# Performance work log

Hardware: AMD Instinct MI355X
Metric: run time of the kernel (lower is better)

Reference implementation:

```python
import jax, jax.numpy as jnp
import numpy as np

V, D, B, L = 100000, 64, 4096, 200

def setup_inputs() -> dict:
    key = jax.random.key(0)
    ks = jax.random.split(key, 10)
    s = 0.05  # keep activations in a sane range for sigmoid
    return {
        "item_ids": jax.random.randint(ks[0], (B,), 0, V),
        "history": jax.random.randint(ks[1], (B, L), 0, V),
        "hist_len": jax.random.randint(ks[2], (B,), 1, L + 1),
        "emb_table": jax.random.normal(ks[3], (V, D), jnp.float32) * s,
        "aW1": jax.random.normal(ks[4], (3 * D, D), jnp.float32) * s,
        "ab1": jnp.zeros((D,), jnp.float32),
        "aW2": jax.random.normal(ks[5], (D, 1), jnp.float32) * s,
        "ab2": jnp.zeros((1,), jnp.float32),
        "fW1": jax.random.normal(ks[6], (3 * D, 128), jnp.float32) * s,
        "fb1": jnp.zeros((128,), jnp.float32),
        "fW2": jax.random.normal(ks[7], (128, 64), jnp.float32) * s,
        "fb2": jnp.zeros((64,), jnp.float32),
        "fW3": jax.random.normal(ks[8], (64, 1), jnp.float32) * s,
        "fb3": jnp.zeros((1,), jnp.float32),
    }

def reference(item_ids, history, hist_len, emb_table, aW1, ab1, aW2, ab2,
              fW1, fb1, fW2, fb2, fW3, fb3):
    target = emb_table[item_ids]                      # [B, D]
    hist = emb_table[history]                         # [B, L, D]
    # original pads short histories with zero rows -> zero the padded tail
    mask = (jnp.arange(hist.shape[1])[None, :] < hist_len[:, None]).astype(hist.dtype)
    hist = hist * mask[..., None]
    tgt = jnp.broadcast_to(target[:, None, :], hist.shape)     # [B, L, D]
    # attention_fc takes 3*D features: (hist, target, hist*target)
    feat = jnp.concatenate([hist, tgt, hist * tgt], axis=-1)   # [B, L, 3D]
    h = jax.nn.relu(feat @ aW1 + ab1)                 # [B, L, D]
    scores = (h @ aW2 + ab2)[..., 0]                  # [B, L]
    # faithful to original: softmax over full padded length (no length mask)
    w = jax.nn.softmax(scores, axis=1)
    pooled = jnp.einsum('bl,bld->bd', w, hist)        # [B, D]
    comb = jnp.concatenate([target, pooled, pooled - target], axis=-1)  # [B, 3D]
    z = jax.nn.relu(comb @ fW1 + fb1)
    z = jax.nn.relu(z @ fW2 + fb2)
    return jax.nn.sigmoid(z @ fW3 + fb3)              # [B, 1]
```

## Files before the change

kernel.cpp:

```cpp
#include <hip/hip_runtime.h>
#include <hip/hip_bf16.h>

#define NV 100000
#define ND 64
#define NB 4096
#define NL 200
#define MT 13

typedef __bf16 bf16_t;
typedef __bf16 bf16x8 __attribute__((ext_vector_type(8)));
typedef __bf16 bf16x4 __attribute__((ext_vector_type(4)));
typedef float f32x4 __attribute__((ext_vector_type(4)));

#define TB_ELEMS ((long)NV * ND)
#define TBV (TB_ELEMS / 8)
#define FT1 (128 * 192)
#define FT2 (64 * 128)
#define CVT_TASKS (TBV + FT1 + FT2)

__global__ __launch_bounds__(256)
void cvt_kernel(const float* __restrict__ emb,
                const float* __restrict__ fW1,
                const float* __restrict__ fW2,
                bf16_t* __restrict__ tb,
                bf16_t* __restrict__ fW1T,
                bf16_t* __restrict__ fW2T)
{
    long t = (long)blockIdx.x * 256 + threadIdx.x;
    if (t >= CVT_TASKS) return;
    if (t < TBV) {
        long i = t * 8;
        f32x4 a0 = *(const f32x4*)(emb + i);
        f32x4 a1 = *(const f32x4*)(emb + i + 4);
        bf16x8 o;
#pragma unroll
        for (int j = 0; j < 4; ++j) { o[j] = (bf16_t)a0[j]; o[j + 4] = (bf16_t)a1[j]; }
        *(bf16x8*)(tb + i) = o;
    } else {
        int u = (int)(t - TBV);
        if (u < FT1) {
            int n = u / 192, k = u - n * 192;
            fW1T[u] = (bf16_t)fW1[k * 128 + n];
        } else {
            int u2 = u - FT1;
            int n = u2 >> 7, k = u2 & 127;
            fW2T[u2] = (bf16_t)fW2[k * 64 + n];
        }
    }
}

__global__ __launch_bounds__(512, 4)
void din_kernel1(const int* __restrict__ item_ids,
                 const int* __restrict__ history,
                 const int* __restrict__ hist_len,
                 const float* __restrict__ emb,
                 const bf16_t* __restrict__ tb,
                 const float* __restrict__ aW1,
                 const float* __restrict__ ab1,
                 const float* __restrict__ aW2,
                 const bf16_t* __restrict__ fW1T, const float* __restrict__ fb1,
                 const bf16_t* __restrict__ fW2T, const float* __restrict__ fb2,
                 const float* __restrict__ fW3, const float* __restrict__ fb3,
                 float* __restrict__ out)
{
    __shared__ __align__(16) bf16_t histA[2][208 * 64];
    __shared__ __align__(16) bf16_t wbT[2][64 * 64];
    __shared__ float tgt[2][64];
    __shared__ __align__(16) float scores[2][208];
    __shared__ float wts[2][208];
    __shared__ float pp2[2][512];
    __shared__ float red[2][8];
    __shared__ float cb2[2][64];

    bf16_t* comb16 = (bf16_t*)wbT;
    bf16_t* z1s    = (bf16_t*)wbT + 3200;
    float*  z2f    = (float*)((bf16_t*)wbT + 5376);

    const int b0  = blockIdx.x * 2;
    const int tid = threadIdx.x;
    const int len0 = hist_len[b0];
    const int len1 = hist_len[b0 + 1];

    if (tid < 128) {
        int bx = tid >> 6, d = tid & 63;
        tgt[bx][d] = emb[(long)item_ids[b0 + bx] * ND + d];
    }

    {
        const int p = tid & 1;
        const int s = tid >> 1;
        const int bxA = (s >= 208);
        const int lA  = s - bxA * 208;
        const int lB  = s + 48;
        const int lenA = bxA ? len1 : len0;
        const bool vB = (s < 160);
        const bf16x8 z = (bf16x8)(bf16_t)0.f;
        bf16x8 a0 = z, a1 = z, a2 = z, a3 = z;
        bf16x8 c0 = z, c1 = z, c2 = z, c3 = z;
        if (lA < lenA) {
            const bf16_t* src = tb + (long)history[(long)(b0 + bxA) * NL + lA] * ND + p * 32;
            a0 = *(const bf16x8*)(src);
            a1 = *(const bf16x8*)(src + 8);
            a2 = *(const bf16x8*)(src + 16);
            a3 = *(const bf16x8*)(src + 24);
        }
        if (vB && lB < len1) {
            const bf16_t* src = tb + (long)history[(long)(b0 + 1) * NL + lB] * ND + p * 32;
            c0 = *(const bf16x8*)(src);
            c1 = *(const bf16x8*)(src + 8);
            c2 = *(const bf16x8*)(src + 16);
            c3 = *(const bf16x8*)(src + 24);
        }
        {
            bf16_t* d = &histA[bxA][lA * 64];
            const int S = (lA & 7) << 3;
            *(bf16x8*)&d[(p * 32 +  0) ^ S] = a0;
            *(bf16x8*)&d[(p * 32 +  8) ^ S] = a1;
            *(bf16x8*)&d[(p * 32 + 16) ^ S] = a2;
            *(bf16x8*)&d[(p * 32 + 24) ^ S] = a3;
        }
        if (vB) {
            bf16_t* d = &histA[1][lB * 64];
            const int S = (lB & 7) << 3;
            *(bf16x8*)&d[(p * 32 +  0) ^ S] = c0;
            *(bf16x8*)&d[(p * 32 +  8) ^ S] = c1;
            *(bf16x8*)&d[(p * 32 + 16) ^ S] = c2;
            *(bf16x8*)&d[(p * 32 + 24) ^ S] = c3;
        }
    }

    {
        const int n  = tid & 63;
        const int kp = tid >> 6;
        const long t0 = (long)item_ids[b0] * ND;
        const long t1 = (long)item_ids[b0 + 1] * ND;
        f32x4 tk0a = *(const f32x4*)(emb + t0 + kp * 8);
        f32x4 tk0b = *(const f32x4*)(emb + t0 + kp * 8 + 4);
        f32x4 tk1a = *(const f32x4*)(emb + t1 + kp * 8);
        f32x4 tk1b = *(const f32x4*)(emb + t1 + kp * 8 + 4);
        float cs0 = 0.f, cs1 = 0.f;
        bf16x8 w0v, w1v;
#pragma unroll
        for (int i = 0; i < 8; ++i) {
            int k = kp * 8 + i;
            float tk0 = (i < 4) ? tk0a[i] : tk0b[i - 4];
            float tk1 = (i < 4) ? tk1a[i] : tk1b[i - 4];
            float ah = aW1[k * 64 + n];
            float am = aW1[(64 + k) * 64 + n];
            float ap = aW1[(128 + k) * 64 + n];
            w0v[i] = (bf16_t)(ah + tk0 * ap);
            w1v[i] = (bf16_t)(ah + tk1 * ap);
            cs0 += tk0 * am;
            cs1 += tk1 * am;
        }
        const int S = (n & 7) << 3;
        *(bf16x8*)&wbT[0][n * 64 + ((kp * 8) ^ S)] = w0v;
        *(bf16x8*)&wbT[1][n * 64 + ((kp * 8) ^ S)] = w1v;
        pp2[0][kp * 64 + n] = cs0;
        pp2[1][kp * 64 + n] = cs1;
    }
    __syncthreads();

    if (tid < 128) {
        const int bx = tid >> 6, n = tid & 63;
        float s = ab1[n];
#pragma unroll
        for (int kp = 0; kp < 8; ++kp) s += pp2[bx][kp * 64 + n];
        cb2[bx][n] = s;
    }
    __syncthreads();

    {
        const int wave = tid >> 6;
        const int lane = tid & 63;
        const int bx   = wave & 1;
        const int col  = lane & 15;
        const int quad = lane >> 4;

        bf16x8 afrag[4][2];
#pragma unroll
        for (int nt = 0; nt < 4; ++nt) {
            const int n = nt * 16 + col;
            const int S = (n & 7) << 3;
#pragma unroll
            for (int kb = 0; kb < 2; ++kb)
                afrag[nt][kb] = *(const bf16x8*)&wbT[bx][n * 64 + ((kb * 32 + quad * 8) ^ S)];
        }
        float cv[4][4], a2[4][4];
#pragma unroll
        for (int nt = 0; nt < 4; ++nt)
#pragma unroll
            for (int i = 0; i < 4; ++i) {
                const int no = nt * 16 + quad * 4 + i;
                cv[nt][i] = cb2[bx][no];
                a2[nt][i] = aW2[no];
            }

        for (int mt = (wave >> 1); mt < MT; mt += 4) {
            const int l = mt * 16 + col;
            const int S = (l & 7) << 3;
            const bf16_t* base = &histA[bx][l * 64];
            bf16x8 bf0 = *(const bf16x8*)&base[(     quad * 8) ^ S];
            bf16x8 bf1 = *(const bf16x8*)&base[(32 + quad * 8) ^ S];
            float sc = 0.f;
#pragma unroll
            for (int nt = 0; nt < 4; ++nt) {
                f32x4 acc = {0.f, 0.f, 0.f, 0.f};
                acc = __builtin_amdgcn_mfma_f32_16x16x32_bf16(afrag[nt][0], bf0, acc, 0, 0, 0);
                acc = __builtin_amdgcn_mfma_f32_16x16x32_bf16(afrag[nt][1], bf1, acc, 0, 0, 0);
#pragma unroll
                for (int i = 0; i < 4; ++i) {
                    float h = acc[i] + cv[nt][i];
                    h = h > 0.f ? h : 0.f;
                    sc += h * a2[nt][i];
                }
            }
            sc += __shfl_xor(sc, 16, 64);
            sc += __shfl_xor(sc, 32, 64);
            if (quad == 0) scores[bx][mt * 16 + col] = sc;
        }
    }
    __syncthreads();

    {
        const int bx = tid >> 8, t = tid & 255;
        float s = (t < NL) ? scores[bx][t] : -1e30f;
        float m = s;
        for (int off = 32; off > 0; off >>= 1) m = fmaxf(m, __shfl_xor(m, off, 64));
        if ((t & 63) == 0) red[bx][t >> 6] = m;
        __syncthreads();
        m = fmaxf(fmaxf(red[bx][0], red[bx][1]), fmaxf(red[bx][2], red[bx][3]));
        float e = (t < NL) ? __expf(s - m) : 0.f;
        if (t < NL) wts[bx][t] = e;
        else if (t < 208) wts[bx][t] = 0.f;
        float ss = e;
        for (int off = 32; off > 0; off >>= 1) ss += __shfl_xor(ss, off, 64);
        if ((t & 63) == 0) red[bx][4 + (t >> 6)] = ss;
        __syncthreads();
    }

    {
        const int bx = tid >> 8, t = tid & 255;
        const int c = t & 15;
        const int g = t >> 4;
        const int w4 = (tid >> 6) & 3;
        const float rtot = 1.f / (red[bx][4] + red[bx][5] + red[bx][6] + red[bx][7]);
        f32x4 acc = {0.f, 0.f, 0.f, 0.f};
#pragma unroll
        for (int j = 0; j < 13; ++j) {
            const int l = g + j * 16;
            const float wl = wts[bx][l];
            bf16x4 v = *(const bf16x4*)&histA[bx][l * 64 + ((c * 4) ^ ((l & 7) << 3))];
#pragma unroll
            for (int k = 0; k < 4; ++k) acc[k] += wl * (float)v[k];
        }
#pragma unroll
        for (int k = 0; k < 4; ++k) {
            acc[k] += __shfl_xor(acc[k], 16, 64);
            acc[k] += __shfl_xor(acc[k], 32, 64);
            acc[k] *= rtot;
        }
        if ((tid & 63) < 16) *(f32x4*)&pp2[bx][w4 * 64 + c * 4] = acc;
    }

    bf16x8 bw1[6]; float b1v;
    bf16x8 bw2[4]; float b2v = 0.f;
    {
        const int wave = tid >> 6, lane = tid & 63;
        const int col = lane & 15, quad = lane >> 4;
        const int n = wave * 16 + col;
#pragma unroll
        for (int ks = 0; ks < 6; ++ks)
            bw1[ks] = *(const bf16x8*)&fW1T[(long)n * 192 + ks * 32 + quad * 8];
        b1v = fb1[n];
        if (wave < 4) {
            const int n2 = wave * 16 + col;
#pragma unroll
            for (int ks = 0; ks < 4; ++ks)
                bw2[ks] = *(const bf16x8*)&fW2T[(long)n2 * 128 + ks * 32 + quad * 8];
            b2v = fb2[n2];
        }
    }
    __syncthreads();

    {
        const int bx = tid >> 8, t = tid & 255;
        if (t < 192) {
            const int d = t & 63;
            float v;
            if (t < 64) v = tgt[bx][d];
            else {
                float pl = pp2[bx][d] + pp2[bx][64 + d] + pp2[bx][128 + d] + pp2[bx][192 + d];
                v = (t < 128) ? pl : pl - tgt[bx][d];
            }
            comb16[bx * 200 + t] = (bf16_t)v;
        }
        if (tid >= 384) {
            const bf16x8 z = (bf16x8)(bf16_t)0.f;
            const int u = tid - 384;
#pragma unroll
            for (int s = u; s < 350; s += 128) *(bf16x8*)&comb16[400 + s * 8] = z;
        }
    }
    __syncthreads();

    {
        const int wave = tid >> 6, lane = tid & 63;
        const int col = lane & 15, quad = lane >> 4;
        f32x4 acc = {0.f, 0.f, 0.f, 0.f};
#pragma unroll
        for (int ks = 0; ks < 6; ++ks) {
            bf16x8 a = *(const bf16x8*)&comb16[col * 200 + ks * 32 + quad * 8];
            acc = __builtin_amdgcn_mfma_f32_16x16x32_bf16(a, bw1[ks], acc, 0, 0, 0);
        }
        const int n = wave * 16 + col;
#pragma unroll
        for (int i = 0; i < 4; ++i) {
            const int m = quad * 4 + i;
            float zv = (m < 2) ? fmaxf(acc[i] + b1v, 0.f) : 0.f;
            z1s[m * 136 + n] = (bf16_t)zv;
        }
    }
    __syncthreads();

    {
        const int wave = tid >> 6, lane = tid & 63;
        const int col = lane & 15, quad = lane >> 4;
        if (wave < 4) {
            f32x4 acc = {0.f, 0.f, 0.f, 0.f};
#pragma unroll
            for (int ks = 0; ks < 4; ++ks) {
                bf16x8 a = *(const bf16x8*)&z1s[col * 136 + ks * 32 + quad * 8];
                acc = __builtin_amdgcn_mfma_f32_16x16x32_bf16(a, bw2[ks], acc, 0, 0, 0);
            }
            const int n2 = wave * 16 + col;
#pragma unroll
            for (int i = 0; i < 4; ++i) {
                const int m = quad * 4 + i;
                if (m < 2) z2f[m * 64 + n2] = fmaxf(acc[i] + b2v, 0.f);
            }
        }
    }
    __syncthreads();

    if (tid < 128) {
        const int bx = tid >> 6, j = tid & 63;
        float s = z2f[bx * 64 + j] * fW3[j];
        for (int off = 32; off > 0; off >>= 1) s += __shfl_xor(s, off, 64);
        if (j == 0) out[b0 + bx] = 1.f / (1.f + __expf(-(s + fb3[0])));
    }
}

extern "C" void kernel_launch(void* const* d_in, const int* in_sizes, int n_in,
                              void* d_out, int out_size, void* d_ws, size_t ws_size,
                              hipStream_t stream) {
    const int*   item_ids = (const int*)d_in[0];
    const int*   history  = (const int*)d_in[1];
    const int*   hist_len = (const int*)d_in[2];
    const float* emb      = (const float*)d_in[3];
    const float* aW1      = (const float*)d_in[4];
    const float* ab1      = (const float*)d_in[5];
    const float* aW2      = (const float*)d_in[6];
    const float* fW1      = (const float*)d_in[8];
    const float* fb1      = (const float*)d_in[9];
    const float* fW2      = (const float*)d_in[10];
    const float* fb2      = (const float*)d_in[11];
    const float* fW3      = (const float*)d_in[12];
    const float* fb3      = (const float*)d_in[13];

    bf16_t* tb   = (bf16_t*)d_ws;
    bf16_t* fW1T = tb + TB_ELEMS;
    bf16_t* fW2T = fW1T + FT1;

    cvt_kernel<<<(int)((CVT_TASKS + 255) / 256), 256, 0, stream>>>(emb, fW1, fW2,
                                                                   tb, fW1T, fW2T);
    din_kernel1<<<NB / 2, 512, 0, stream>>>(item_ids, history, hist_len, emb, tb,
                                            aW1, ab1, aW2,
                                            fW1T, fb1, fW2T, fb2, fW3, fb3,
                                            (float*)d_out);
}
```

Baseline: 140.1 us.

## Process one batch row per 256-thread block instead of two per 512-thread block

Restructures the main kernel so each block handles a single sample with 256 threads, launching NB blocks instead of NB/2. Shared memory per block shrinks because the FC scratch buffers are aliased into histA, and the softmax drops one barrier by computing per-wave max and sum and rescaling them afterwards. Biases are folded into the MFMA accumulator initialisation. Each block now does twice the per-thread work in the FC stage, and fewer warps per block may reduce latency hiding within a block, while more, smaller blocks may schedule more flexibly.

```diff
diff --git a/kernel.cpp b/kernel.cpp
--- a/kernel.cpp
+++ b/kernel.cpp
@@ -49,7 +49,7 @@
     }
 }
 
-__global__ __launch_bounds__(512, 4)
+__global__ __launch_bounds__(256, 4)
 void din_kernel1(const int* __restrict__ item_ids,
                  const int* __restrict__ history,
                  const int* __restrict__ hist_len,
@@ -63,65 +63,57 @@
                  const float* __restrict__ fW3, const float* __restrict__ fb3,
                  float* __restrict__ out)
 {
-    __shared__ __align__(16) bf16_t histA[2][208 * 64];
-    __shared__ __align__(16) bf16_t wbT[2][64 * 64];
-    __shared__ float tgt[2][64];
-    __shared__ __align__(16) float scores[2][208];
-    __shared__ float wts[2][208];
-    __shared__ float pp2[2][512];
-    __shared__ float red[2][8];
-    __shared__ float cb2[2][64];
-
-    bf16_t* comb16 = (bf16_t*)wbT;
-    bf16_t* z1s    = (bf16_t*)wbT + 3200;
-    float*  z2f    = (float*)((bf16_t*)wbT + 5376);
-
-    const int b0  = blockIdx.x * 2;
+    __shared__ __align__(16) bf16_t histA[208 * 64];
+    __shared__ __align__(16) bf16_t wbT[64 * 64];
+    __shared__ float tgt[64];
+    __shared__ __align__(16) float scores[208];
+    __shared__ float wts[208];
+    __shared__ float pp[4 * 64];
+    __shared__ float red[8];
+    __shared__ float cb2[64];
+
+    bf16_t* comb16 = histA;
+    bf16_t* z1s    = histA + 3328;
+    float*  z2f    = (float*)(histA + 5504);
+
+    const int b   = blockIdx.x;
     const int tid = threadIdx.x;
-    const int len0 = hist_len[b0];
-    const int len1 = hist_len[b0 + 1];
-
-    if (tid < 128) {
-        int bx = tid >> 6, d = tid & 63;
-        tgt[bx][d] = emb[(long)item_ids[b0 + bx] * ND + d];
-    }
-
-    {
-        const int p = tid & 1;
-        const int s = tid >> 1;
-        const int bxA = (s >= 208);
-        const int lA  = s - bxA * 208;
-        const int lB  = s + 48;
-        const int lenA = bxA ? len1 : len0;
-        const bool vB = (s < 160);
+    const int len = hist_len[b];
+
+    if (tid < 64) tgt[tid] = emb[(long)item_ids[b] * ND + tid];
+
+    {
+        const int p  = tid & 1;
+        const int l0 = tid >> 1;
+        const int l1 = l0 + 128;
         const bf16x8 z = (bf16x8)(bf16_t)0.f;
         bf16x8 a0 = z, a1 = z, a2 = z, a3 = z;
         bf16x8 c0 = z, c1 = z, c2 = z, c3 = z;
-        if (lA < lenA) {
-            const bf16_t* src = tb + (long)history[(long)(b0 + bxA) * NL + lA] * ND + p * 32;
-            a0 = *(const bf16x8*)(src);
-            a1 = *(const bf16x8*)(src + 8);
-            a2 = *(const bf16x8*)(src + 16);
-            a3 = *(const bf16x8*)(src + 24);
-        }
-        if (vB && lB < len1) {
-            const bf16_t* src = tb + (long)history[(long)(b0 + 1) * NL + lB] * ND + p * 32;
-            c0 = *(const bf16x8*)(src);
-            c1 = *(const bf16x8*)(src + 8);
-            c2 = *(const bf16x8*)(src + 16);
-            c3 = *(const bf16x8*)(src + 24);
+        if (l0 < len) {
+            const bf16_t* s = tb + (long)history[(long)b * NL + l0] * ND + p * 32;
+            a0 = *(const bf16x8*)(s);
+            a1 = *(const bf16x8*)(s + 8);
+            a2 = *(const bf16x8*)(s + 16);
+            a3 = *(const bf16x8*)(s + 24);
+        }
+        if (l1 < len) {
+            const bf16_t* s = tb + (long)history[(long)b * NL + l1] * ND + p * 32;
+            c0 = *(const bf16x8*)(s);
+            c1 = *(const bf16x8*)(s + 8);
+            c2 = *(const bf16x8*)(s + 16);
+            c3 = *(const bf16x8*)(s + 24);
         }
         {
-            bf16_t* d = &histA[bxA][lA * 64];
-            const int S = (lA & 7) << 3;
+            bf16_t* d = &histA[l0 * 64];
+            const int S = (l0 & 7) << 3;
             *(bf16x8*)&d[(p * 32 +  0) ^ S] = a0;
             *(bf16x8*)&d[(p * 32 +  8) ^ S] = a1;
             *(bf16x8*)&d[(p * 32 + 16) ^ S] = a2;
             *(bf16x8*)&d[(p * 32 + 24) ^ S] = a3;
         }
-        if (vB) {
-            bf16_t* d = &histA[1][lB * 64];
-            const int S = (lB & 7) << 3;
+        if (l1 < 208) {
+            bf16_t* d = &histA[l1 * 64];
+            const int S = (l1 & 7) << 3;
             *(bf16x8*)&d[(p * 32 +  0) ^ S] = c0;
             *(bf16x8*)&d[(p * 32 +  8) ^ S] = c1;
             *(bf16x8*)&d[(p * 32 + 16) ^ S] = c2;
@@ -132,48 +124,39 @@
     {
         const int n  = tid & 63;
         const int kp = tid >> 6;
-        const long t0 = (long)item_ids[b0] * ND;
-        const long t1 = (long)item_ids[b0 + 1] * ND;
-        f32x4 tk0a = *(const f32x4*)(emb + t0 + kp * 8);
-        f32x4 tk0b = *(const f32x4*)(emb + t0 + kp * 8 + 4);
-        f32x4 tk1a = *(const f32x4*)(emb + t1 + kp * 8);
-        f32x4 tk1b = *(const f32x4*)(emb + t1 + kp * 8 + 4);
-        float cs0 = 0.f, cs1 = 0.f;
+        const long t0 = (long)item_ids[b] * ND;
+        f32x4 tka = *(const f32x4*)(emb + t0 + kp * 16);
+        f32x4 tkb = *(const f32x4*)(emb + t0 + kp * 16 + 4);
+        f32x4 tkc = *(const f32x4*)(emb + t0 + kp * 16 + 8);
+        f32x4 tkd = *(const f32x4*)(emb + t0 + kp * 16 + 12);
+        float csum = 0.f;
         bf16x8 w0v, w1v;
 #pragma unroll
-        for (int i = 0; i < 8; ++i) {
-            int k = kp * 8 + i;
-            float tk0 = (i < 4) ? tk0a[i] : tk0b[i - 4];
-            float tk1 = (i < 4) ? tk1a[i] : tk1b[i - 4];
+        for (int i = 0; i < 16; ++i) {
+            int k = kp * 16 + i;
+            float tk = (i < 4) ? tka[i] : (i < 8) ? tkb[i - 4]
+                     : (i < 12) ? tkc[i - 8] : tkd[i - 12];
             float ah = aW1[k * 64 + n];
             float am = aW1[(64 + k) * 64 + n];
             float ap = aW1[(128 + k) * 64 + n];
-            w0v[i] = (bf16_t)(ah + tk0 * ap);
-            w1v[i] = (bf16_t)(ah + tk1 * ap);
-            cs0 += tk0 * am;
-            cs1 += tk1 * am;
+            float w  = ah + tk * ap;
+            if (i < 8) w0v[i] = (bf16_t)w; else w1v[i - 8] = (bf16_t)w;
+            csum += tk * am;
         }
         const int S = (n & 7) << 3;
-        *(bf16x8*)&wbT[0][n * 64 + ((kp * 8) ^ S)] = w0v;
-        *(bf16x8*)&wbT[1][n * 64 + ((kp * 8) ^ S)] = w1v;
-        pp2[0][kp * 64 + n] = cs0;
-        pp2[1][kp * 64 + n] = cs1;
-    }
-    __syncthreads();
-
-    if (tid < 128) {
-        const int bx = tid >> 6, n = tid & 63;
-        float s = ab1[n];
-#pragma unroll
-        for (int kp = 0; kp < 8; ++kp) s += pp2[bx][kp * 64 + n];
-        cb2[bx][n] = s;
-    }
+        *(bf16x8*)&wbT[n * 64 + ((kp * 16    ) ^ S)] = w0v;
+        *(bf16x8*)&wbT[n * 64 + ((kp * 16 + 8) ^ S)] = w1v;
+        pp[kp * 64 + n] = csum;
+    }
+    __syncthreads();
+
+    if (tid < 64)
+        cb2[tid] = ab1[tid] + pp[tid] + pp[64 + tid] + pp[128 + tid] + pp[192 + tid];
     __syncthreads();
 
     {
         const int wave = tid >> 6;
         const int lane = tid & 63;
-        const int bx   = wave & 1;
         const int col  = lane & 15;
         const int quad = lane >> 4;
 
@@ -184,7 +167,7 @@
             const int S = (n & 7) << 3;
 #pragma unroll
             for (int kb = 0; kb < 2; ++kb)
-                afrag[nt][kb] = *(const bf16x8*)&wbT[bx][n * 64 + ((kb * 32 + quad * 8) ^ S)];
+                afrag[nt][kb] = *(const bf16x8*)&wbT[n * 64 + ((kb * 32 + quad * 8) ^ S)];
         }
         float cv[4][4], a2[4][4];
 #pragma unroll
@@ -192,65 +175,66 @@
 #pragma unroll
             for (int i = 0; i < 4; ++i) {
                 const int no = nt * 16 + quad * 4 + i;
-                cv[nt][i] = cb2[bx][no];
+                cv[nt][i] = cb2[no];
                 a2[nt][i] = aW2[no];
             }
 
-        for (int mt = (wave >> 1); mt < MT; mt += 4) {
+        for (int mt = wave; mt < MT; mt += 4) {
             const int l = mt * 16 + col;
             const int S = (l & 7) << 3;
-            const bf16_t* base = &histA[bx][l * 64];
+            const bf16_t* base = &histA[l * 64];
             bf16x8 bf0 = *(const bf16x8*)&base[(     quad * 8) ^ S];
             bf16x8 bf1 = *(const bf16x8*)&base[(32 + quad * 8) ^ S];
             float sc = 0.f;
 #pragma unroll
             for (int nt = 0; nt < 4; ++nt) {
-                f32x4 acc = {0.f, 0.f, 0.f, 0.f};
+                f32x4 acc = {cv[nt][0], cv[nt][1], cv[nt][2], cv[nt][3]};
                 acc = __builtin_amdgcn_mfma_f32_16x16x32_bf16(afrag[nt][0], bf0, acc, 0, 0, 0);
                 acc = __builtin_amdgcn_mfma_f32_16x16x32_bf16(afrag[nt][1], bf1, acc, 0, 0, 0);
 #pragma unroll
                 for (int i = 0; i < 4; ++i) {
-                    float h = acc[i] + cv[nt][i];
-                    h = h > 0.f ? h : 0.f;
+                    float h = acc[i] > 0.f ? acc[i] : 0.f;
                     sc += h * a2[nt][i];
                 }
             }
             sc += __shfl_xor(sc, 16, 64);
             sc += __shfl_xor(sc, 32, 64);
-            if (quad == 0) scores[bx][mt * 16 + col] = sc;
-        }
-    }
-    __syncthreads();
-
-    {
-        const int bx = tid >> 8, t = tid & 255;
-        float s = (t < NL) ? scores[bx][t] : -1e30f;
+            if (quad == 0) scores[mt * 16 + col] = sc;
+        }
+    }
+    __syncthreads();
+
+    {
+        float s = (tid < NL) ? scores[tid] : -1e30f;
         float m = s;
         for (int off = 32; off > 0; off >>= 1) m = fmaxf(m, __shfl_xor(m, off, 64));
-        if ((t & 63) == 0) red[bx][t >> 6] = m;
-        __syncthreads();
-        m = fmaxf(fmaxf(red[bx][0], red[bx][1]), fmaxf(red[bx][2], red[bx][3]));
-        float e = (t < NL) ? __expf(s - m) : 0.f;
-        if (t < NL) wts[bx][t] = e;
-        else if (t < 208) wts[bx][t] = 0.f;
+        float e = (tid < NL) ? __expf(s - m) : 0.f;
+        if (tid < NL) wts[tid] = e;
+        else if (tid < 208) wts[tid] = 0.f;
         float ss = e;
         for (int off = 32; off > 0; off >>= 1) ss += __shfl_xor(ss, off, 64);
-        if ((t & 63) == 0) red[bx][4 + (t >> 6)] = ss;
-        __syncthreads();
-    }
-
-    {
-        const int bx = tid >> 8, t = tid & 255;
-        const int c = t & 15;
-        const int g = t >> 4;
-        const int w4 = (tid >> 6) & 3;
-        const float rtot = 1.f / (red[bx][4] + red[bx][5] + red[bx][6] + red[bx][7]);
+        if ((tid & 63) == 0) { red[tid >> 6] = m; red[4 + (tid >> 6)] = ss; }
+    }
+    __syncthreads();
+
+    {
+        const int c  = tid & 15;
+        const int g  = tid >> 4;
+        const int w4 = tid >> 6;
+        const float m0 = red[0], m1 = red[1], m2 = red[2], m3 = red[3];
+        const float mg = fmaxf(fmaxf(m0, m1), fmaxf(m2, m3));
+        float sc0 = __expf(m0 - mg), sc1 = __expf(m1 - mg);
+        float sc2 = __expf(m2 - mg), sc3 = __expf(m3 - mg);
+        const float rtot = 1.f / (sc0 * red[4] + sc1 * red[5] +
+                                  sc2 * red[6] + sc3 * red[7]);
+        sc0 *= rtot; sc1 *= rtot; sc2 *= rtot; sc3 *= rtot;
         f32x4 acc = {0.f, 0.f, 0.f, 0.f};
 #pragma unroll
         for (int j = 0; j < 13; ++j) {
             const int l = g + j * 16;
-            const float wl = wts[bx][l];
-            bf16x4 v = *(const bf16x4*)&histA[bx][l * 64 + ((c * 4) ^ ((l & 7) << 3))];
+            const float scj = (j < 4) ? sc0 : (j < 8) ? sc1 : (j < 12) ? sc2 : sc3;
+            const float wl = wts[l] * scj;
+            bf16x4 v = *(const bf16x4*)&histA[l * 64 + ((c * 4) ^ ((l & 7) << 3))];
 #pragma unroll
             for (int k = 0; k < 4; ++k) acc[k] += wl * (float)v[k];
         }
@@ -258,48 +242,47 @@
         for (int k = 0; k < 4; ++k) {
             acc[k] += __shfl_xor(acc[k], 16, 64);
             acc[k] += __shfl_xor(acc[k], 32, 64);
-            acc[k] *= rtot;
-        }
-        if ((tid & 63) < 16) *(f32x4*)&pp2[bx][w4 * 64 + c * 4] = acc;
-    }
-
-    bf16x8 bw1[6]; float b1v;
-    bf16x8 bw2[4]; float b2v = 0.f;
+        }
+        if ((tid & 63) < 16) *(f32x4*)&pp[w4 * 64 + c * 4] = acc;
+    }
+
+    bf16x8 bw1[2][6]; float b1v[2];
+    bf16x8 bw2[4];    float b2v;
     {
         const int wave = tid >> 6, lane = tid & 63;
         const int col = lane & 15, quad = lane >> 4;
-        const int n = wave * 16 + col;
-#pragma unroll
-        for (int ks = 0; ks < 6; ++ks)
-            bw1[ks] = *(const bf16x8*)&fW1T[(long)n * 192 + ks * 32 + quad * 8];
-        b1v = fb1[n];
-        if (wave < 4) {
-            const int n2 = wave * 16 + col;
-#pragma unroll
-            for (int ks = 0; ks < 4; ++ks)
-                bw2[ks] = *(const bf16x8*)&fW2T[(long)n2 * 128 + ks * 32 + quad * 8];
-            b2v = fb2[n2];
-        }
-    }
-    __syncthreads();
-
-    {
-        const int bx = tid >> 8, t = tid & 255;
-        if (t < 192) {
-            const int d = t & 63;
+#pragma unroll
+        for (int tt = 0; tt < 2; ++tt) {
+            const int n = (wave * 2 + tt) * 16 + col;
+#pragma unroll
+            for (int ks = 0; ks < 6; ++ks)
+                bw1[tt][ks] = *(const bf16x8*)&fW1T[(long)n * 192 + ks * 32 + quad * 8];
+            b1v[tt] = fb1[n];
+        }
+        const int n2 = wave * 16 + col;
+#pragma unroll
+        for (int ks = 0; ks < 4; ++ks)
+            bw2[ks] = *(const bf16x8*)&fW2T[(long)n2 * 128 + ks * 32 + quad * 8];
+        b2v = fb2[n2];
+    }
+    __syncthreads();
+
+    {
+        if (tid < 192) {
+            const int d = tid & 63;
             float v;
-            if (t < 64) v = tgt[bx][d];
+            if (tid < 64) v = tgt[d];
             else {
-                float pl = pp2[bx][d] + pp2[bx][64 + d] + pp2[bx][128 + d] + pp2[bx][192 + d];
-                v = (t < 128) ? pl : pl - tgt[bx][d];
-            }
-            comb16[bx * 200 + t] = (bf16_t)v;
-        }
-        if (tid >= 384) {
-            const bf16x8 z = (bf16x8)(bf16_t)0.f;
-            const int u = tid - 384;
-#pragma unroll
-            for (int s = u; s < 350; s += 128) *(bf16x8*)&comb16[400 + s * 8] = z;
+                float pl = pp[d] + pp[64 + d] + pp[128 + d] + pp[192 + d];
+                v = (tid < 128) ? pl : pl - tgt[d];
+            }
+            comb16[tid] = (bf16_t)v;
+        }
+        const bf16x8 z = (bf16x8)(bf16_t)0.f;
+        for (int s = tid; s < 360; s += 256) {
+            const int m = s / 24 + 1;
+            const int c = (s % 24) * 8;
+            *(bf16x8*)&comb16[m * 200 + c] = z;
         }
     }
     __syncthreads();
@@ -307,18 +290,21 @@
     {
         const int wave = tid >> 6, lane = tid & 63;
         const int col = lane & 15, quad = lane >> 4;
-        f32x4 acc = {0.f, 0.f, 0.f, 0.f};
-#pragma unroll
-        for (int ks = 0; ks < 6; ++ks) {
-            bf16x8 a = *(const bf16x8*)&comb16[col * 200 + ks * 32 + quad * 8];
-            acc = __builtin_amdgcn_mfma_f32_16x16x32_bf16(a, bw1[ks], acc, 0, 0, 0);
-        }
-        const int n = wave * 16 + col;
-#pragma unroll
-        for (int i = 0; i < 4; ++i) {
-            const int m = quad * 4 + i;
-            float zv = (m < 2) ? fmaxf(acc[i] + b1v, 0.f) : 0.f;
-            z1s[m * 136 + n] = (bf16_t)zv;
+#pragma unroll
+        for (int tt = 0; tt < 2; ++tt) {
+            f32x4 acc = {b1v[tt], b1v[tt], b1v[tt], b1v[tt]};
+#pragma unroll
+            for (int ks = 0; ks < 6; ++ks) {
+                bf16x8 a = *(const bf16x8*)&comb16[col * 200 + ks * 32 + quad * 8];
+                acc = __builtin_amdgcn_mfma_f32_16x16x32_bf16(a, bw1[tt][ks], acc, 0, 0, 0);
+            }
+            const int n = (wave * 2 + tt) * 16 + col;
+#pragma unroll
+            for (int i = 0; i < 4; ++i) {
+                const int m = quad * 4 + i;
+                float zv = (m == 0) ? fmaxf(acc[i], 0.f) : 0.f;
+                z1s[m * 136 + n] = (bf16_t)zv;
+            }
         }
     }
     __syncthreads();
@@ -326,28 +312,21 @@
     {
         const int wave = tid >> 6, lane = tid & 63;
         const int col = lane & 15, quad = lane >> 4;
-        if (wave < 4) {
-            f32x4 acc = {0.f, 0.f, 0.f, 0.f};
-#pragma unroll
-            for (int ks = 0; ks < 4; ++ks) {
-                bf16x8 a = *(const bf16x8*)&z1s[col * 136 + ks * 32 + quad * 8];
-                acc = __builtin_amdgcn_mfma_f32_16x16x32_bf16(a, bw2[ks], acc, 0, 0, 0);
-            }
-            const int n2 = wave * 16 + col;
-#pragma unroll
-            for (int i = 0; i < 4; ++i) {
-                const int m = quad * 4 + i;
-                if (m < 2) z2f[m * 64 + n2] = fmaxf(acc[i] + b2v, 0.f);
-            }
-        }
-    }
-    __syncthreads();
-
-    if (tid < 128) {
-        const int bx = tid >> 6, j = tid & 63;
-        float s = z2f[bx * 64 + j] * fW3[j];
+        f32x4 acc = {b2v, b2v, b2v, b2v};
+#pragma unroll
+        for (int ks = 0; ks < 4; ++ks) {
+            bf16x8 a = *(const bf16x8*)&z1s[col * 136 + ks * 32 + quad * 8];
+            acc = __builtin_amdgcn_mfma_f32_16x16x32_bf16(a, bw2[ks], acc, 0, 0, 0);
+        }
+        const int n2 = wave * 16 + col;
+        if (quad == 0) z2f[n2] = fmaxf(acc[0], 0.f);
+    }
+    __syncthreads();
+
+    if (tid < 64) {
+        float s = z2f[tid] * fW3[tid];
         for (int off = 32; off > 0; off >>= 1) s += __shfl_xor(s, off, 64);
-        if (j == 0) out[b0 + bx] = 1.f / (1.f + __expf(-(s + fb3[0])));
+        if (tid == 0) out[b] = 1.f / (1.f + __expf(-(s + fb3[0])));
     }
 }
 
@@ -374,8 +353,8 @@
 
     cvt_kernel<<<(int)((CVT_TASKS + 255) / 256), 256, 0, stream>>>(emb, fW1, fW2,
                                                                    tb, fW1T, fW2T);
-    din_kernel1<<<NB / 2, 512, 0, stream>>>(item_ids, history, hist_len, emb, tb,
-                                            aW1, ab1, aW2,
-                                            fW1T, fb1, fW2T, fb2, fW3, fb3,
-                                            (float*)d_out);
+    din_kernel1<<<NB, 256, 0, stream>>>(item_ids, history, hist_len, emb, tb,
+                                        aW1, ab1, aW2,
+                                        fW1T, fb1, fW2T, fb2, fW3, fb3,
+                                        (float*)d_out);
 }
```

Result: slower. 154.4 us (+10.2%).
